# Optimization experiments

Measured on AMD Instinct MI355X. Metric: run time of the kernel, lower is better.

Reference implementation:

```python
import jax, jax.numpy as jnp
import numpy as np

L, M, K = 13, 12, 5
ODD_KS = tuple(range(1, K + 1, 2))  # (1, 3, 5) -> n_odd_order = 3
NK = len(ODD_KS)


def setup_inputs() -> dict:
    key = jax.random.key(0)
    k1, k2, k3, k4 = jax.random.split(key, 4)
    B, T = 16, 8192
    x = jax.random.normal(k1, (B, T, 2), dtype=jnp.float32)
    h_0 = jnp.zeros((B, 16), dtype=jnp.float32)  # unused by forward (API compat)
    A_kl = jax.random.normal(k2, (L, NK), dtype=jnp.float32) * 0.1
    B_klm = jax.random.normal(k3, (L, M, NK), dtype=jnp.float32) * 0.1
    C_klm = jax.random.normal(k4, (L, M, NK), dtype=jnp.float32) * 0.1
    return {"x": x, "h_0": h_0, "A_kl": A_kl, "B_klm": B_klm, "C_klm": C_klm}


def _gmp_forward(x, A_kl, B_klm, C_klm):
    # x: [B, T, 2] real/imag -> complex signal
    Bsz, T, _ = x.shape
    xc = jax.lax.complex(x[..., 0], x[..., 1])  # [B, T]

    # Circular window indices (equivalent to torch cat+unfold in the original).
    t = jnp.arange(T)[:, None, None]
    l = jnp.arange(L)[None, :, None]
    m = jnp.arange(M + 1)[None, None, :]
    # 2nd term pads with the LAST (L+M-1) samples at the front -> index shift back
    idx2 = (t + l + m - (L + M - 1)) % T  # [T, L, M+1]
    # 3rd term pads with the FIRST (L+M-1) samples at the end -> forward wrap
    idx3 = (t + l + m) % T                # [T, L, M+1]

    x2 = xc[:, idx2]  # [B, T, L, M+1] complex
    x3 = xc[:, idx3]  # [B, T, L, M+1] complex
    # First-term window x[t-(L-1)+l] equals the m=M element of the 2nd-term window.
    x1 = x2[..., -1]  # [B, T, L]

    # --- term 1: sum_{l,k} A[l,k] * x1 * |x1|^k ---
    a1 = jnp.abs(x1)                                        # [B,T,L]
    p1 = jnp.stack([a1 ** k for k in ODD_KS], axis=-1)       # [B,T,L,NK] real
    c1 = jnp.einsum('btlk,lk->btl', p1, A_kl)                # real coefficient
    term1 = jnp.sum(x1 * c1, axis=-1)                        # [B,T] complex

    # --- term 2: sum_{l,m,k} B[l,m,k] * x2[...,M] * |x2[...,m]|^k ---
    a2 = jnp.abs(x2[..., :-1])                               # [B,T,L,M]
    p2 = jnp.stack([a2 ** k for k in ODD_KS], axis=-1)       # [B,T,L,M,NK]
    c2 = jnp.einsum('btlmk,lmk->btl', p2, B_klm)             # sum over m,k too
    term2 = jnp.sum(x1 * c2, axis=-1)                        # multiplier is x2[...,-1]==x1

    # --- term 3: same structure with forward-lag windows and C ---
    x3_last = x3[..., -1]                                    # [B,T,L]
    a3 = jnp.abs(x3[..., :-1])                               # [B,T,L,M]
    p3 = jnp.stack([a3 ** k for k in ODD_KS], axis=-1)       # [B,T,L,M,NK]
    c3 = jnp.einsum('btlmk,lmk->btl', p3, C_klm)
    term3 = jnp.sum(x3_last * c3, axis=-1)

    s = term1 + term2 + term3                                # [B,T] complex
    return jnp.stack([jnp.real(s), jnp.imag(s)], axis=-1)    # [B,T,2] float32


def reference(x, h_0, A_kl, B_klm, C_klm):
    # h_0 is accepted but unused, matching the torch module.
    return _gmp_forward(x, A_kl, B_klm, C_klm)
```

## Files before the change

kernel.cpp:

```cpp
#include <hip/hip_runtime.h>
#include <math.h>

#define LL   13
#define MM   12
#define NKK  3
#define BLOCK 256
#define HALO  24
#define WIN  (BLOCK + 2*HALO)


__global__ __launch_bounds__(BLOCK)
void gmp_kernel(const float* __restrict__ x,
                const float* __restrict__ Ac,
                const float* __restrict__ Bc,
                const float* __restrict__ Cc,
                float* __restrict__ out,
                int T, int tilesPerB)
{
    __shared__ float4 sP[WIN];
    __shared__ float2 sZ[WIN];

    const int tid = threadIdx.x;
    const int b   = blockIdx.x / tilesPerB;
    const int t0  = (blockIdx.x % tilesPerB) * BLOCK;

    const float* xb = x + (size_t)b * T * 2;

    for (int i = tid; i < WIN; i += BLOCK) {
        int t = t0 - HALO + i;
        if (t < 0)  t += T;
        if (t >= T) t -= T;
        float re = xb[2 * t], im = xb[2 * t + 1];
        float a2 = re * re + im * im;
        float a  = sqrtf(a2);
        sZ[i] = make_float2(re, im);
        sP[i] = make_float4(a, a * a2, a * a2 * a2, 0.0f);
    }
    __syncthreads();

    float cB[LL], cC[LL];
    #pragma unroll
    for (int l = 0; l < LL; ++l) {
        const float4 p = sP[tid + l + 12];
        cB[l] = Ac[l * NKK + 0] * p.x
              + Ac[l * NKK + 1] * p.y
              + Ac[l * NKK + 2] * p.z;
        cC[l] = 0.0f;
    }

    #pragma unroll
    for (int d = 0; d < LL + MM - 1; ++d) {
        const float4 p = sP[tid + d];
        const float4 q = sP[tid + d + HALO];
        #pragma unroll
        for (int l = 0; l < LL; ++l) {
            const int m = d - l;
            if (m >= 0 && m < MM) {
                const float* bp = Bc + (l * MM + m) * NKK;
                cB[l] += bp[0] * p.x + bp[1] * p.y + bp[2] * p.z;
                const float* cp = Cc + (l * MM + m) * NKK;
                cC[l] += cp[0] * q.x + cp[1] * q.y + cp[2] * q.z;
            }
        }
    }

    float sr = 0.0f, si = 0.0f;
    #pragma unroll
    for (int l = 0; l < LL; ++l) {
        const float2 z1 = sZ[tid + l + 12];
        const float2 z3 = sZ[tid + l + 36];
        sr += z1.x * cB[l] + z3.x * cC[l];
        si += z1.y * cB[l] + z3.y * cC[l];
    }

    const int t = t0 + tid;
    if (t < T) {
        out[((size_t)b * T + t) * 2 + 0] = sr;
        out[((size_t)b * T + t) * 2 + 1] = si;
    }
}

extern "C" void kernel_launch(void* const* d_in, const int* in_sizes, int n_in,
                              void* d_out, int out_size, void* d_ws, size_t ws_size,
                              hipStream_t stream)
{
    const float* x  = (const float*)d_in[0];
    const float* Ac = (const float*)d_in[2];
    const float* Bc = (const float*)d_in[3];
    const float* Cc = (const float*)d_in[4];
    float* out = (float*)d_out;

    const int Bsz = in_sizes[1] / 16;
    const int T   = in_sizes[0] / (2 * Bsz);
    const int tilesPerB = (T + BLOCK - 1) / BLOCK;

    dim3 grid(Bsz * tilesPerB);
    dim3 block(BLOCK);
    gmp_kernel<<<grid, block, 0, stream>>>(x, Ac, Bc, Cc, out, T, tilesPerB);
}
```

Measured before the change: 73.94 us.

## Split lag-diagonal accumulation across four thread slices with shared-memory reduction

Each block now covers a 64-sample tile and uses four 64-thread slices. Each slice accumulates a quarter of the 24 lag diagonals, and the partial complex sums are reduced through shared memory before one slice writes the output. This spreads each output's work over more threads and gives four times as many blocks, raising parallelism for a workload of only 131k outputs. In exchange it adds a second barrier, a reduction step, halo reloads per smaller tile, and warp-uniform branching on the slice index.

```diff
diff --git a/kernel.cpp b/kernel.cpp
--- a/kernel.cpp
+++ b/kernel.cpp
@@ -1,13 +1,34 @@
 #include <hip/hip_runtime.h>
 #include <math.h>
 
-#define LL   13
-#define MM   12
-#define NKK  3
-#define BLOCK 256
+#define LL    13
+#define MM    12
+#define NKK   3
+#define TILE  64
+#define SLICES 4
+#define BLOCK (TILE * SLICES)
 #define HALO  24
-#define WIN  (BLOCK + 2*HALO)
+#define WIN   (TILE + 2 * HALO)
+#define DTOT  (LL + MM - 1)
+#define DPS   (DTOT / SLICES)
 
+
+#define SLICE_BODY(S)                                                   \
+  { _Pragma("unroll")                                                   \
+    for (int d = DPS * (S); d < DPS * (S) + DPS; ++d) {                 \
+      const float4 p = sP[i + d];                                       \
+      const float4 q = sP[i + d + HALO];                                \
+      _Pragma("unroll")                                                 \
+      for (int l = 0; l < LL; ++l) {                                    \
+        const int m = d - l;                                            \
+        if (m >= 0 && m < MM) {              \
+          const float* bp = Bc + (l * MM + m) * NKK;                    \
+          cB[l] += bp[0] * p.x + bp[1] * p.y + bp[2] * p.z;             \
+          const float* cp = Cc + (l * MM + m) * NKK;                    \
+          cC[l] += cp[0] * q.x + cp[1] * q.y + cp[2] * q.z;             \
+        }                                                               \
+      }                                                                 \
+    } }
 
 __global__ __launch_bounds__(BLOCK)
 void gmp_kernel(const float* __restrict__ x,
@@ -19,64 +40,68 @@
 {
     __shared__ float4 sP[WIN];
     __shared__ float2 sZ[WIN];
+    __shared__ float2 sRed[SLICES][TILE];
 
     const int tid = threadIdx.x;
+    const int i   = tid & (TILE - 1);
+    const int s   = tid >> 6;
     const int b   = blockIdx.x / tilesPerB;
-    const int t0  = (blockIdx.x % tilesPerB) * BLOCK;
+    const int t0  = (blockIdx.x % tilesPerB) * TILE;
 
     const float* xb = x + (size_t)b * T * 2;
 
-    for (int i = tid; i < WIN; i += BLOCK) {
-        int t = t0 - HALO + i;
+    for (int j = tid; j < WIN; j += BLOCK) {
+        int t = t0 - HALO + j;
         if (t < 0)  t += T;
         if (t >= T) t -= T;
         float re = xb[2 * t], im = xb[2 * t + 1];
         float a2 = re * re + im * im;
         float a  = sqrtf(a2);
-        sZ[i] = make_float2(re, im);
-        sP[i] = make_float4(a, a * a2, a * a2 * a2, 0.0f);
+        sZ[j] = make_float2(re, im);
+        sP[j] = make_float4(a, a * a2, a * a2 * a2, 0.0f);
     }
     __syncthreads();
 
     float cB[LL], cC[LL];
     #pragma unroll
-    for (int l = 0; l < LL; ++l) {
-        const float4 p = sP[tid + l + 12];
-        cB[l] = Ac[l * NKK + 0] * p.x
-              + Ac[l * NKK + 1] * p.y
-              + Ac[l * NKK + 2] * p.z;
-        cC[l] = 0.0f;
-    }
+    for (int l = 0; l < LL; ++l) { cB[l] = 0.0f; cC[l] = 0.0f; }
 
-    #pragma unroll
-    for (int d = 0; d < LL + MM - 1; ++d) {
-        const float4 p = sP[tid + d];
-        const float4 q = sP[tid + d + HALO];
+    if (s == 0) {
+        SLICE_BODY(0)
         #pragma unroll
         for (int l = 0; l < LL; ++l) {
-            const int m = d - l;
-            if (m >= 0 && m < MM) {
-                const float* bp = Bc + (l * MM + m) * NKK;
-                cB[l] += bp[0] * p.x + bp[1] * p.y + bp[2] * p.z;
-                const float* cp = Cc + (l * MM + m) * NKK;
-                cC[l] += cp[0] * q.x + cp[1] * q.y + cp[2] * q.z;
-            }
+            const float4 p = sP[i + l + 12];
+            cB[l] += Ac[l * NKK + 0] * p.x
+                   + Ac[l * NKK + 1] * p.y
+                   + Ac[l * NKK + 2] * p.z;
         }
+    } else if (s == 1) {
+        SLICE_BODY(1)
+    } else if (s == 2) {
+        SLICE_BODY(2)
+    } else {
+        SLICE_BODY(3)
     }
 
     float sr = 0.0f, si = 0.0f;
     #pragma unroll
     for (int l = 0; l < LL; ++l) {
-        const float2 z1 = sZ[tid + l + 12];
-        const float2 z3 = sZ[tid + l + 36];
+        const float2 z1 = sZ[i + l + 12];
+        const float2 z3 = sZ[i + l + 36];
         sr += z1.x * cB[l] + z3.x * cC[l];
         si += z1.y * cB[l] + z3.y * cC[l];
     }
+    sRed[s][i] = make_float2(sr, si);
+    __syncthreads();
 
-    const int t = t0 + tid;
-    if (t < T) {
-        out[((size_t)b * T + t) * 2 + 0] = sr;
-        out[((size_t)b * T + t) * 2 + 1] = si;
+    if (s == 0) {
+        const float2 r0 = sRed[0][i], r1 = sRed[1][i];
+        const float2 r2 = sRed[2][i], r3 = sRed[3][i];
+        const int t = t0 + i;
+        if (t < T) {
+            out[((size_t)b * T + t) * 2 + 0] = r0.x + r1.x + r2.x + r3.x;
+            out[((size_t)b * T + t) * 2 + 1] = r0.y + r1.y + r2.y + r3.y;
+        }
     }
 }
 
@@ -92,7 +117,7 @@
 
     const int Bsz = in_sizes[1] / 16;
     const int T   = in_sizes[0] / (2 * Bsz);
-    const int tilesPerB = (T + BLOCK - 1) / BLOCK;
+    const int tilesPerB = (T + TILE - 1) / TILE;
 
     dim3 grid(Bsz * tilesPerB);
     dim3 block(BLOCK);
```

New measurement: 82.87 us. 12.1% more time.
